# Performance work log

Measured on AMD Instinct MI355X. Metric: run time of the kernel, lower is better.

Reference implementation:

```python
import jax, jax.numpy as jnp
import numpy as np

NUM_NEIGHBORS = 1000

def setup_inputs() -> dict:
    key = jax.random.key(0)
    k1, k2, k3 = jax.random.split(key, 3)
    N, R, H, O = 1024, 100000, 512, 256
    x = jax.random.normal(k1, (N, H), dtype=jnp.float32)
    ref_x = jax.random.normal(k2, (R, H), dtype=jnp.float32)
    ref_y = jax.random.normal(k3, (R, O), dtype=jnp.float32)
    return {"x": x, "ref_x": ref_x, "ref_y": ref_y}

def reference(x, ref_x, ref_y):
    # encoder1 modeled as identity (x is the encoded embedding)
    xn = x / jnp.linalg.norm(x, axis=-1, keepdims=True)          # [N, H]
    rn = ref_x / jnp.linalg.norm(ref_x, axis=-1, keepdims=True)  # [R, H]
    sim = jnp.einsum('nh,rh->nr', xn, rn)                        # [N, R] cosine sims
    knn_vals, knn_idx = jax.lax.top_k(sim, NUM_NEIGHBORS)        # [N, K]
    weight = jax.nn.softmax(knn_vals, axis=1)                    # [N, K]
    neigh_y = ref_y[knn_idx]                                     # [N, K, O]
    pred_y = jnp.einsum('nko,nk->no', neigh_y, weight)           # [N, O]
    return pred_y
```

## Files before the change

kernel.cpp:

```cpp
#include <hip/hip_runtime.h>
#include <hip/hip_bf16.h>
#include <hip/hip_fp16.h>
#include <stdint.h>

#define NQ 1024
#define NR 100000
#define NH 512
#define NO 256
#define NK 1000
#define NBINS 4096
#define DEF_CAP 1024
#define CND_CAP 768
#define DELTA 2.0e-3f

typedef __attribute__((ext_vector_type(8))) short bf16x8;
typedef __attribute__((ext_vector_type(4))) float f32x4;
typedef __attribute__((address_space(3))) void lds_void;
typedef const __attribute__((address_space(1))) void glb_void;

static __device__ inline uint32_t pack_bf16_trunc(float lo, float hi) {
    return __builtin_amdgcn_perm(__float_as_uint(hi), __float_as_uint(lo), 0x07060302u);
}

__global__ __launch_bounds__(256) void conv_norm_kernel(const float* __restrict__ src,
                                                        int rows,
                                                        ushort* __restrict__ dst_bf,
                                                        double* __restrict__ inv_out)
{
    const int wave = threadIdx.x >> 6;
    const int lane = threadIdx.x & 63;
    const int row  = blockIdx.x * 4 + wave;
    if (row >= rows) return;
    const float* p = src + (size_t)row * NH + lane * 8;
    float4 v0 = *(const float4*)p;
    float4 v1 = *(const float4*)(p + 4);
    double s = (double)v0.x * v0.x + (double)v0.y * v0.y
             + (double)v0.z * v0.z + (double)v0.w * v0.w
             + (double)v1.x * v1.x + (double)v1.y * v1.y
             + (double)v1.z * v1.z + (double)v1.w * v1.w;
    uint4 pk;
    pk.x = pack_bf16_trunc(v0.x, v0.y);
    pk.y = pack_bf16_trunc(v0.z, v0.w);
    pk.z = pack_bf16_trunc(v1.x, v1.y);
    pk.w = pack_bf16_trunc(v1.z, v1.w);
    *(uint4*)(dst_bf + (size_t)row * NH + lane * 8) = pk;
    #pragma unroll
    for (int off = 32; off > 0; off >>= 1) s += __shfl_down(s, off, 64);
    if (lane == 0) inv_out[row] = 1.0 / sqrt(s);
}

__global__ __launch_bounds__(256) void conv_ry_kernel(const float* __restrict__ ry,
                                                      __half* __restrict__ ryh)
{
    const int wave = threadIdx.x >> 6;
    const int lane = threadIdx.x & 63;
    const int row  = blockIdx.x * 4 + wave;
    float4 v = *(const float4*)(ry + (size_t)row * NO + lane * 4);
    __half2 h01 = __floats2half2_rn(v.x, v.y);
    __half2 h23 = __floats2half2_rn(v.z, v.w);
    uint2 pk;
    pk.x = __builtin_bit_cast(uint32_t, h01);
    pk.y = __builtin_bit_cast(uint32_t, h23);
    *(uint2*)(ryh + (size_t)row * NO + lane * 4) = pk;
}

__global__ __launch_bounds__(256) void gemm_kernel(const ushort* __restrict__ xbf,
                                                   const ushort* __restrict__ rxbf,
                                                   const double* __restrict__ xinv,
                                                   const double* __restrict__ rinv,
                                                   __half* __restrict__ sim)
{
    __shared__ ushort a_lds[128 * 64];
    __shared__ ushort b_lds[128 * 64];
    const int bid = blockIdx.x;
    const int nt  = (bid & 7) + 8 * (bid >> 6);
    const int mt  = (bid >> 3) & 7;
    if (nt >= (NR + 127) / 128) return;
    const int m0 = mt * 128;
    const int r0 = nt * 128;

    const int tid  = threadIdx.x;
    const int lane = tid & 63;
    const int wave = tid >> 6;
    const int wq = (wave >> 1) * 64;
    const int wr = (wave & 1) * 64;

    f32x4 acc[4][4];
    #pragma unroll
    for (int i = 0; i < 4; ++i)
        #pragma unroll
        for (int j = 0; j < 4; ++j)
            #pragma unroll
            for (int r = 0; r < 4; ++r) acc[i][j][r] = 0.0f;

    const int srow  = lane >> 3;
    const int chunk = (lane & 7) ^ (srow & 7);

    for (int kt = 0; kt < NH; kt += 64) {
        #pragma unroll
        for (int ii = 0; ii < 4; ++ii) {
            const int inst = wave * 4 + ii;
            const int row  = inst * 8 + srow;
            const ushort* ga = xbf + (size_t)(m0 + row) * NH + kt + chunk * 8;
            __builtin_amdgcn_global_load_lds((glb_void*)ga,
                (lds_void*)(a_lds + inst * 512), 16, 0, 0);
            int rr = r0 + row; if (rr > NR - 1) rr = NR - 1;
            const ushort* gb = rxbf + (size_t)rr * NH + kt + chunk * 8;
            __builtin_amdgcn_global_load_lds((glb_void*)gb,
                (lds_void*)(b_lds + inst * 512), 16, 0, 0);
        }
        __syncthreads();
        #pragma unroll
        for (int kc = 0; kc < 2; ++kc) {
            const int c  = kc * 4 + (lane >> 4);
            const int px = (c ^ (lane & 7)) * 8;
            bf16x8 af[4], bfr[4];
            #pragma unroll
            for (int i = 0; i < 4; ++i)
                af[i] = *(const bf16x8*)&a_lds[(wq + i * 16 + (lane & 15)) * 64 + px];
            #pragma unroll
            for (int j = 0; j < 4; ++j)
                bfr[j] = *(const bf16x8*)&b_lds[(wr + j * 16 + (lane & 15)) * 64 + px];
            #pragma unroll
            for (int i = 0; i < 4; ++i)
                #pragma unroll
                for (int j = 0; j < 4; ++j)
                    acc[i][j] = __builtin_amdgcn_mfma_f32_16x16x32_bf16(af[i], bfr[j], acc[i][j], 0, 0, 0);
        }
        __syncthreads();
    }

    float xi[4][4];
    #pragma unroll
    for (int i = 0; i < 4; ++i) {
        int mb = m0 + wq + i * 16 + (lane >> 4) * 4;
        #pragma unroll
        for (int r = 0; r < 4; ++r) xi[i][r] = (float)xinv[mb + r];
    }
    #pragma unroll
    for (int j = 0; j < 4; ++j) {
        int nn = r0 + wr + j * 16 + (lane & 15);
        if (nn < NR) {
            float rv = (float)rinv[nn];
            #pragma unroll
            for (int i = 0; i < 4; ++i) {
                int mb = m0 + wq + i * 16 + (lane >> 4) * 4;
                #pragma unroll
                for (int r = 0; r < 4; ++r)
                    sim[(size_t)(mb + r) * NR + nn] = __float2half(acc[i][j][r] * xi[i][r] * rv);
            }
        }
    }
}

__global__ __launch_bounds__(256) void hist_collect_kernel(const __half* __restrict__ sim,
                                                           uint32_t* __restrict__ def_cnt,
                                                           uint32_t* __restrict__ cand_cnt,
                                                           float* __restrict__ def_val,
                                                           uint32_t* __restrict__ def_idx,
                                                           uint32_t* __restrict__ cand_idx)
{
    __shared__ uint32_t h[NBINS];
    __shared__ uint32_t ps[256];
    __shared__ float s_thi, s_tlo;
    __shared__ uint32_t s_dc, s_cc;
    const int n = blockIdx.x, tid = threadIdx.x;
    for (int b = tid; b < NBINS; b += 256) h[b] = 0u;
    __syncthreads();
    const uint4* row8 = (const uint4*)(sim + (size_t)n * NR);
    for (int i8 = tid; i8 < NR / 8; i8 += 256) {
        uint4 v = row8[i8];
        uint32_t ws[4] = {v.x, v.y, v.z, v.w};
        #pragma unroll
        for (int c = 0; c < 4; ++c) {
            float2 f = __half22float2(__builtin_bit_cast(__half2, ws[c]));
            int b0 = (int)((f.x + 1.0f) * 2048.0f); b0 = min(max(b0, 0), NBINS - 1); atomicAdd(&h[b0], 1u);
            int b1 = (int)((f.y + 1.0f) * 2048.0f); b1 = min(max(b1, 0), NBINS - 1); atomicAdd(&h[b1], 1u);
        }
    }
    __syncthreads();
    uint32_t cs = 0;
    #pragma unroll 4
    for (int b = 0; b < 16; ++b) cs += h[tid * 16 + b];
    ps[tid] = cs;
    __syncthreads();
    if (tid == 0) {
        uint32_t acc = 0; int tc = 0;
        for (int t2 = 255; t2 >= 0; --t2) {
            if (acc + ps[t2] >= (uint32_t)NK) { tc = t2; break; }
            acc += ps[t2];
        }
        int bstar = tc * 16;
        for (int b = tc * 16 + 15; b >= tc * 16; --b) {
            acc += h[b];
            if (acc >= (uint32_t)NK) { bstar = b; break; }
        }
        s_thi = (float)(bstar + 1) * (1.0f / 2048.0f) - 1.0f + DELTA;
        s_tlo = (float)bstar * (1.0f / 2048.0f) - 1.0f - DELTA;
        s_dc = 0u; s_cc = 0u;
    }
    __syncthreads();
    const float thi = s_thi, tlo = s_tlo;
    for (int i8 = tid; i8 < NR / 8; i8 += 256) {
        uint4 v = row8[i8];
        uint32_t ws[4] = {v.x, v.y, v.z, v.w};
        const int base = i8 * 8;
        #pragma unroll
        for (int c = 0; c < 4; ++c) {
            float2 f = __half22float2(__builtin_bit_cast(__half2, ws[c]));
            float sv[2] = {f.x, f.y};
            #pragma unroll
            for (int d = 0; d < 2; ++d) {
                float s = sv[d];
                if (s > thi) {
                    uint32_t p = atomicAdd(&s_dc, 1u);
                    if (p < DEF_CAP) {
                        def_val[(size_t)n * DEF_CAP + p] = s;
                        def_idx[(size_t)n * DEF_CAP + p] = (uint32_t)(base + c * 2 + d);
                    }
                } else if (s >= tlo) {
                    uint32_t p = atomicAdd(&s_cc, 1u);
                    if (p < CND_CAP) cand_idx[(size_t)n * CND_CAP + p] = (uint32_t)(base + c * 2 + d);
                }
            }
        }
    }
    __syncthreads();
    if (tid == 0) {
        def_cnt[n]  = s_dc < DEF_CAP ? s_dc : DEF_CAP;
        cand_cnt[n] = s_cc < CND_CAP ? s_cc : CND_CAP;
    }
}

__global__ __launch_bounds__(1024) void final_kernel(const float* __restrict__ x,
                                                     const float* __restrict__ rx,
                                                     const __half* __restrict__ ryh,
                                                     const double* __restrict__ xinv,
                                                     const double* __restrict__ rinv,
                                                     const uint32_t* __restrict__ def_cnt,
                                                     const uint32_t* __restrict__ cand_cnt,
                                                     const float* __restrict__ def_val,
                                                     const uint32_t* __restrict__ def_idx,
                                                     const uint32_t* __restrict__ cand_idx,
                                                     float* __restrict__ out)
{
    const int n = blockIdx.x, tid = threadIdx.x;
    const int lane = tid & 63, wave = tid >> 6;
    const int hl = lane & 31;
    const int slot = tid >> 5;
    __shared__ double   cvd[CND_CAP];
    __shared__ uint32_t ci[CND_CAP];
    __shared__ float    sel_w[DEF_CAP];
    __shared__ uint32_t sel_idx[DEF_CAP];
    __shared__ float    red[16];
    __shared__ float    s_r[32][264];
    __shared__ uint32_t s_sel;

    const int ca = (int)def_cnt[n];
    const int cb = (int)cand_cnt[n];
    int t = NK - ca; if (t > cb) t = cb; if (t < 0) t = 0;

    for (int j = tid; j < ca; j += 1024) {
        sel_w[j]   = def_val[(size_t)n * DEF_CAP + j];
        sel_idx[j] = def_idx[(size_t)n * DEF_CAP + j];
    }
    for (int j = tid; j < cb; j += 1024)
        ci[j] = cand_idx[(size_t)n * CND_CAP + j];
    if (tid == 0) s_sel = 0u;
    __syncthreads();

    const float* xr = x + (size_t)n * NH;
    float4 xv[4];
    #pragma unroll
    for (int i = 0; i < 4; ++i) xv[i] = *(const float4*)(xr + hl * 4 + i * 128);
    const double xin = xinv[n];

    for (int j = slot; j < cb; j += 64) {
        const int j2 = j + 32;
        const bool has2 = (j2 < cb);
        const float* r1 = rx + (size_t)ci[j] * NH;
        const float* r2 = rx + (size_t)ci[has2 ? j2 : j] * NH;
        float4 ra[4], rb[4];
        #pragma unroll
        for (int i = 0; i < 4; ++i) ra[i] = *(const float4*)(r1 + hl * 4 + i * 128);
        #pragma unroll
        for (int i = 0; i < 4; ++i) rb[i] = *(const float4*)(r2 + hl * 4 + i * 128);
        double sA = 0.0, sB = 0.0;
        #pragma unroll
        for (int i = 0; i < 4; ++i) {
            sA += (double)xv[i].x * ra[i].x + (double)xv[i].y * ra[i].y
                + (double)xv[i].z * ra[i].z + (double)xv[i].w * ra[i].w;
            sB += (double)xv[i].x * rb[i].x + (double)xv[i].y * rb[i].y
                + (double)xv[i].z * rb[i].z + (double)xv[i].w * rb[i].w;
        }
        #pragma unroll
        for (int off = 16; off > 0; off >>= 1) {
            sA += __shfl_down(sA, off, 64);
            sB += __shfl_down(sB, off, 64);
        }
        if (hl == 0) {
            cvd[j] = (sA * xin) * rinv[ci[j]];
            if (has2) cvd[j2] = (sB * xin) * rinv[ci[j2]];
        }
    }
    __syncthreads();

    if (tid < cb) {
        double vj = cvd[tid]; uint32_t ij = ci[tid];
        int rank = 0;
        for (int i = 0; i < cb; ++i) {
            double vi = cvd[i];
            rank += (vi > vj) || (vi == vj && ci[i] < ij);
        }
        if (rank < t) {
            uint32_t p = atomicAdd(&s_sel, 1u);
            sel_w[ca + p]   = (float)vj;
            sel_idx[ca + p] = ij;
        }
    }
    __syncthreads();
    const int M = ca + t;

    float lm = -3.0e38f;
    for (int k = tid; k < M; k += 1024) lm = fmaxf(lm, sel_w[k]);
    #pragma unroll
    for (int off = 32; off > 0; off >>= 1) lm = fmaxf(lm, __shfl_xor(lm, off, 64));
    if (lane == 0) red[wave] = lm;
    __syncthreads();
    float mx = red[0];
    #pragma unroll
    for (int w2 = 1; w2 < 16; ++w2) mx = fmaxf(mx, red[w2]);
    __syncthreads();

    float ls = 0.f;
    for (int k = tid; k < M; k += 1024) {
        float w = expf(sel_w[k] - mx);
        sel_w[k] = w;
        ls += w;
    }
    #pragma unroll
    for (int off = 32; off > 0; off >>= 1) ls += __shfl_xor(ls, off, 64);
    if (lane == 0) red[wave] = ls;
    __syncthreads();
    float wsum = red[0];
    #pragma unroll
    for (int w2 = 1; w2 < 16; ++w2) wsum += red[w2];

    float acc[8];
    #pragma unroll
    for (int c = 0; c < 8; ++c) acc[c] = 0.f;
    for (int k = slot; k < M; k += 64) {
        const int k2 = k + 32;
        const bool has2 = (k2 < M);
        const uint4 v1 = *(const uint4*)(ryh + (size_t)sel_idx[k] * NO + hl * 8);
        const uint4 v2 = *(const uint4*)(ryh + (size_t)sel_idx[has2 ? k2 : k] * NO + hl * 8);
        const float w1 = sel_w[k];
        const float w2 = has2 ? sel_w[k2] : 0.f;
        float2 f;
        f = __half22float2(__builtin_bit_cast(__half2, v1.x)); acc[0] = fmaf(w1, f.x, acc[0]); acc[1] = fmaf(w1, f.y, acc[1]);
        f = __half22float2(__builtin_bit_cast(__half2, v1.y)); acc[2] = fmaf(w1, f.x, acc[2]); acc[3] = fmaf(w1, f.y, acc[3]);
        f = __half22float2(__builtin_bit_cast(__half2, v1.z)); acc[4] = fmaf(w1, f.x, acc[4]); acc[5] = fmaf(w1, f.y, acc[5]);
        f = __half22float2(__builtin_bit_cast(__half2, v1.w)); acc[6] = fmaf(w1, f.x, acc[6]); acc[7] = fmaf(w1, f.y, acc[7]);
        f = __half22float2(__builtin_bit_cast(__half2, v2.x)); acc[0] = fmaf(w2, f.x, acc[0]); acc[1] = fmaf(w2, f.y, acc[1]);
        f = __half22float2(__builtin_bit_cast(__half2, v2.y)); acc[2] = fmaf(w2, f.x, acc[2]); acc[3] = fmaf(w2, f.y, acc[3]);
        f = __half22float2(__builtin_bit_cast(__half2, v2.z)); acc[4] = fmaf(w2, f.x, acc[4]); acc[5] = fmaf(w2, f.y, acc[5]);
        f = __half22float2(__builtin_bit_cast(__half2, v2.w)); acc[6] = fmaf(w2, f.x, acc[6]); acc[7] = fmaf(w2, f.y, acc[7]);
    }
    *(float4*)&s_r[slot][hl * 8 + 0] = make_float4(acc[0], acc[1], acc[2], acc[3]);
    *(float4*)&s_r[slot][hl * 8 + 4] = make_float4(acc[4], acc[5], acc[6], acc[7]);
    __syncthreads();
    if (tid < 256) {
        float s = 0.f;
        #pragma unroll
        for (int p = 0; p < 32; ++p) s += s_r[p][tid];
        out[(size_t)n * NO + tid] = s / wsum;
    }
}

extern "C" void kernel_launch(void* const* d_in, const int* in_sizes, int n_in,
                              void* d_out, int out_size, void* d_ws, size_t ws_size,
                              hipStream_t stream)
{
    const float* x  = (const float*)d_in[0];
    const float* rx = (const float*)d_in[1];
    const float* ry = (const float*)d_in[2];
    float* out = (float*)d_out;

    char* ws = (char*)d_ws;
    __half*   simh     = (__half*)(ws);
    ushort*   rxbf     = (ushort*)(ws + 204800000ull);
    __half*   ryh      = (__half*)(ws + 307200000ull);
    ushort*   xbf      = (ushort*)(ws + 358400000ull);
    double*   rinv     = (double*)(ws + 359448576ull);
    double*   xinv     = (double*)(ws + 360248576ull);
    uint32_t* def_cnt  = (uint32_t*)(ws + 360256768ull);
    uint32_t* cand_cnt = (uint32_t*)(ws + 360260864ull);
    float*    def_val  = (float*)(ws + 360264960ull);
    uint32_t* def_idx  = (uint32_t*)(ws + 364459264ull);
    uint32_t* cand_idx = (uint32_t*)(ws + 368653568ull);

    conv_norm_kernel<<<NQ / 4, 256, 0, stream>>>(x, NQ, xbf, xinv);
    conv_norm_kernel<<<NR / 4, 256, 0, stream>>>(rx, NR, rxbf, rinv);
    conv_ry_kernel<<<NR / 4, 256, 0, stream>>>(ry, ryh);
    gemm_kernel<<<6272, 256, 0, stream>>>(xbf, rxbf, xinv, rinv, simh);
    hist_collect_kernel<<<NQ, 256, 0, stream>>>(simh, def_cnt, cand_cnt,
                                                def_val, def_idx, cand_idx);
    final_kernel<<<NQ, 1024, 0, stream>>>(x, rx, ryh, xinv, rinv, def_cnt, cand_cnt,
                                          def_val, def_idx, cand_idx, out);
}
```

Before: 926.1 us.

## Restructure similarity GEMM into 256x256 tiles with a 4-stage async LDS pipeline

Rewrites the bf16 similarity GEMM to use 512-thread blocks computing 256x256 output tiles over 32-wide K slices. Each slice is staged into a 4-deep ring of dynamic LDS buffers via global_load_lds, prefetched three stages ahead, with explicit vmcnt waits and s_setprio around the MFMA bursts. Blocks are remapped for L2 locality. The intent is to hide global-load latency behind MFMA work and raise arithmetic intensity per LDS load. The cost is 128KB of LDS per block, which limits occupancy to one block per CU, plus higher register pressure from the 8x4 accumulator tile.

```diff
diff --git a/kernel.cpp b/kernel.cpp
--- a/kernel.cpp
+++ b/kernel.cpp
@@ -64,90 +64,132 @@
     *(uint2*)(ryh + (size_t)row * NO + lane * 4) = pk;
 }
 
-__global__ __launch_bounds__(256) void gemm_kernel(const ushort* __restrict__ xbf,
-                                                   const ushort* __restrict__ rxbf,
-                                                   const double* __restrict__ xinv,
-                                                   const double* __restrict__ rinv,
-                                                   __half* __restrict__ sim)
-{
-    __shared__ ushort a_lds[128 * 64];
-    __shared__ ushort b_lds[128 * 64];
+__global__ __launch_bounds__(512, 2) void gemm_kernel(const ushort* __restrict__ xbf,
+                                                      const ushort* __restrict__ rxbf,
+                                                      const double* __restrict__ xinv,
+                                                      const double* __restrict__ rinv,
+                                                      __half* __restrict__ sim)
+{
+    extern __shared__ ushort lds[];
     const int bid = blockIdx.x;
-    const int nt  = (bid & 7) + 8 * (bid >> 6);
-    const int mt  = (bid >> 3) & 7;
-    if (nt >= (NR + 127) / 128) return;
-    const int m0 = mt * 128;
-    const int r0 = nt * 128;
-
-    const int tid  = threadIdx.x;
-    const int lane = tid & 63;
-    const int wave = tid >> 6;
-    const int wq = (wave >> 1) * 64;
-    const int wr = (wave & 1) * 64;
-
-    f32x4 acc[4][4];
-    #pragma unroll
-    for (int i = 0; i < 4; ++i)
-        #pragma unroll
-        for (int j = 0; j < 4; ++j)
+    const int wg  = (bid & 7) * 196 + (bid >> 3);
+    const int mt  = wg & 3;
+    const int nt  = wg >> 2;
+    const int r0  = nt * 256;
+    if (r0 >= NR) return;
+    const int m0  = mt * 256;
+
+    const int tid    = threadIdx.x;
+    const int lane   = tid & 63;
+    const int wave   = tid >> 6;
+    const int warp_m = wave >> 2;
+    const int warp_n = wave & 3;
+
+    const ushort* srcA[2];
+    const ushort* srcB[2];
+    uint32_t dstOff[2];
+    #pragma unroll
+    for (int r = 0; r < 2; ++r) {
+        const int c   = r * 512 + tid;
+        const int j   = c >> 3;
+        const int v   = (c & 7) ^ (j & 7);
+        const int row = (j << 1) | (v >> 2);
+        const int kc  = v & 3;
+        srcA[r] = xbf + (size_t)(m0 + row) * NH + kc * 8;
+        int rb = r0 + row; if (rb > NR - 1) rb = NR - 1;
+        srcB[r] = rxbf + (size_t)rb * NH + kc * 8;
+        dstOff[r] = (uint32_t)((r * 512 + wave * 64) * 8);
+    }
+
+    const int kcF = lane >> 4;
+    uint32_t aOff[8], bOff[4];
+    #pragma unroll
+    for (int m = 0; m < 8; ++m) {
+        const int row = warp_m * 128 + m * 16 + (lane & 15);
+        const int j   = row >> 1;
+        const int pos = (((row & 1) << 2) | kcF) ^ (j & 7);
+        aOff[m] = (uint32_t)(j * 64 + pos * 8);
+    }
+    #pragma unroll
+    for (int n = 0; n < 4; ++n) {
+        const int row = warp_n * 64 + n * 16 + (lane & 15);
+        const int j   = row >> 1;
+        const int pos = (((row & 1) << 2) | kcF) ^ (j & 7);
+        bOff[n] = (uint32_t)(j * 64 + pos * 8);
+    }
+
+    f32x4 acc[8][4];
+    #pragma unroll
+    for (int m = 0; m < 8; ++m)
+        #pragma unroll
+        for (int n = 0; n < 4; ++n)
             #pragma unroll
-            for (int r = 0; r < 4; ++r) acc[i][j][r] = 0.0f;
-
-    const int srow  = lane >> 3;
-    const int chunk = (lane & 7) ^ (srow & 7);
-
-    for (int kt = 0; kt < NH; kt += 64) {
-        #pragma unroll
-        for (int ii = 0; ii < 4; ++ii) {
-            const int inst = wave * 4 + ii;
-            const int row  = inst * 8 + srow;
-            const ushort* ga = xbf + (size_t)(m0 + row) * NH + kt + chunk * 8;
-            __builtin_amdgcn_global_load_lds((glb_void*)ga,
-                (lds_void*)(a_lds + inst * 512), 16, 0, 0);
-            int rr = r0 + row; if (rr > NR - 1) rr = NR - 1;
-            const ushort* gb = rxbf + (size_t)rr * NH + kt + chunk * 8;
-            __builtin_amdgcn_global_load_lds((glb_void*)gb,
-                (lds_void*)(b_lds + inst * 512), 16, 0, 0);
-        }
-        __syncthreads();
-        #pragma unroll
-        for (int kc = 0; kc < 2; ++kc) {
-            const int c  = kc * 4 + (lane >> 4);
-            const int px = (c ^ (lane & 7)) * 8;
-            bf16x8 af[4], bfr[4];
+            for (int r = 0; r < 4; ++r) acc[m][n][r] = 0.0f;
+
+#define STAGE(kh) do {                                                          \
+        const uint32_t sbase_ = (uint32_t)(((kh) & 3) * 8192);                  \
+        _Pragma("unroll")                                                       \
+        for (int r_ = 0; r_ < 2; ++r_)                                          \
+            __builtin_amdgcn_global_load_lds((glb_void*)(srcA[r_] + (kh) * 32), \
+                (lds_void*)(lds + sbase_ + dstOff[r_]), 16, 0, 0);              \
+        _Pragma("unroll")                                                       \
+        for (int r_ = 0; r_ < 2; ++r_)                                          \
+            __builtin_amdgcn_global_load_lds((glb_void*)(srcB[r_] + (kh) * 32), \
+                (lds_void*)(lds + 32768 + sbase_ + dstOff[r_]), 16, 0, 0);      \
+    } while (0)
+
+    STAGE(0); STAGE(1); STAGE(2);
+
+    #pragma unroll
+    for (int s = 0; s < 16; ++s) {
+        if (s + 3 < 16) STAGE(s + 3);
+        if (s <= 12)      asm volatile("s_waitcnt vmcnt(12)" ::: "memory");
+        else if (s == 13) asm volatile("s_waitcnt vmcnt(8)"  ::: "memory");
+        else if (s == 14) asm volatile("s_waitcnt vmcnt(4)"  ::: "memory");
+        else              asm volatile("s_waitcnt vmcnt(0)"  ::: "memory");
+        __builtin_amdgcn_s_barrier();
+        asm volatile("" ::: "memory");
+
+        const ushort* as = lds + (s & 3) * 8192;
+        const ushort* bs = as + 32768;
+        bf16x8 af[8], bf[4];
+        #pragma unroll
+        for (int m = 0; m < 8; ++m) af[m] = *(const bf16x8*)(as + aOff[m]);
+        #pragma unroll
+        for (int n = 0; n < 4; ++n) bf[n] = *(const bf16x8*)(bs + bOff[n]);
+
+        __builtin_amdgcn_s_setprio(1);
+        #pragma unroll
+        for (int m = 0; m < 8; ++m)
             #pragma unroll
-            for (int i = 0; i < 4; ++i)
-                af[i] = *(const bf16x8*)&a_lds[(wq + i * 16 + (lane & 15)) * 64 + px];
+            for (int n = 0; n < 4; ++n)
+                acc[m][n] = __builtin_amdgcn_mfma_f32_16x16x32_bf16(af[m], bf[n], acc[m][n], 0, 0, 0);
+        __builtin_amdgcn_s_setprio(0);
+
+        asm volatile("" ::: "memory");
+        __builtin_amdgcn_s_barrier();
+        asm volatile("" ::: "memory");
+    }
+#undef STAGE
+
+    float xi[8][4];
+    #pragma unroll
+    for (int m = 0; m < 8; ++m) {
+        const int mb = m0 + warp_m * 128 + m * 16 + (lane >> 4) * 4;
+        #pragma unroll
+        for (int r = 0; r < 4; ++r) xi[m][r] = (float)xinv[mb + r];
+    }
+    #pragma unroll
+    for (int n = 0; n < 4; ++n) {
+        const int nn = r0 + warp_n * 64 + n * 16 + (lane & 15);
+        if (nn < NR) {
+            const float rv = (float)rinv[nn];
             #pragma unroll
-            for (int j = 0; j < 4; ++j)
-                bfr[j] = *(const bf16x8*)&b_lds[(wr + j * 16 + (lane & 15)) * 64 + px];
-            #pragma unroll
-            for (int i = 0; i < 4; ++i)
-                #pragma unroll
-                for (int j = 0; j < 4; ++j)
-                    acc[i][j] = __builtin_amdgcn_mfma_f32_16x16x32_bf16(af[i], bfr[j], acc[i][j], 0, 0, 0);
-        }
-        __syncthreads();
-    }
-
-    float xi[4][4];
-    #pragma unroll
-    for (int i = 0; i < 4; ++i) {
-        int mb = m0 + wq + i * 16 + (lane >> 4) * 4;
-        #pragma unroll
-        for (int r = 0; r < 4; ++r) xi[i][r] = (float)xinv[mb + r];
-    }
-    #pragma unroll
-    for (int j = 0; j < 4; ++j) {
-        int nn = r0 + wr + j * 16 + (lane & 15);
-        if (nn < NR) {
-            float rv = (float)rinv[nn];
-            #pragma unroll
-            for (int i = 0; i < 4; ++i) {
-                int mb = m0 + wq + i * 16 + (lane >> 4) * 4;
+            for (int m = 0; m < 8; ++m) {
+                const int mb = m0 + warp_m * 128 + m * 16 + (lane >> 4) * 4;
                 #pragma unroll
                 for (int r = 0; r < 4; ++r)
-                    sim[(size_t)(mb + r) * NR + nn] = __float2half(acc[i][j][r] * xi[i][r] * rv);
+                    sim[(size_t)(mb + r) * NR + nn] = __float2half(acc[m][n][r] * xi[m][r] * rv);
             }
         }
     }
@@ -399,10 +441,17 @@
     uint32_t* def_idx  = (uint32_t*)(ws + 364459264ull);
     uint32_t* cand_idx = (uint32_t*)(ws + 368653568ull);
 
+    static bool lds_attr_set = false;
+    if (!lds_attr_set) {
+        hipFuncSetAttribute((const void*)gemm_kernel,
+                            hipFuncAttributeMaxDynamicSharedMemorySize, 131072);
+        lds_attr_set = true;
+    }
+
     conv_norm_kernel<<<NQ / 4, 256, 0, stream>>>(x, NQ, xbf, xinv);
     conv_norm_kernel<<<NR / 4, 256, 0, stream>>>(rx, NR, rxbf, rinv);
     conv_ry_kernel<<<NR / 4, 256, 0, stream>>>(ry, ryh);
-    gemm_kernel<<<6272, 256, 0, stream>>>(xbf, rxbf, xinv, rinv, simh);
+    gemm_kernel<<<1568, 512, 131072, stream>>>(xbf, rxbf, xinv, rinv, simh);
     hist_collect_kernel<<<NQ, 256, 0, stream>>>(simh, def_cnt, cand_cnt,
                                                 def_val, def_idx, cand_idx);
     final_kernel<<<NQ, 1024, 0, stream>>>(x, rx, ryh, xinv, rinv, def_cnt, cand_cnt,
```

Measured after the change: 928.5 us. About the same (+0.3%).
